# Optimization experiments

Hardware: AMD Instinct MI355X
Metric: run time of the kernel (lower is better)

## Reference

```python
import jax, jax.numpy as jnp
import numpy as np

T, N, D_OBS = 32, 32, 64
HID, HEADS, MEM, N_ACT = 512, 4, 128, 16
SECTIONS = [HEADS * HID, HEADS, HID, 1, HID, HID, HEADS, 1, 1, 3 * HEADS]
XI = sum(SECTIONS)


def setup_inputs() -> dict:
    key = jax.random.key(0)
    ks = jax.random.split(key, 8)
    s = 0.02
    return {
        "inputs": jax.random.normal(ks[0], (T, N, D_OBS), jnp.float32),
        "w_ih": jax.random.normal(ks[1], (3 * HID, D_OBS), jnp.float32) * s,
        "w_hh": jax.random.normal(ks[2], (3 * HID, HID), jnp.float32) * s,
        "b_ih": jnp.zeros((3 * HID,), jnp.float32),
        "b_hh": jnp.zeros((3 * HID,), jnp.float32),
        "Wf": jax.random.normal(ks[3], (XI, HID), jnp.float32) * s,
        "bf": jnp.zeros((XI,), jnp.float32),
        "Wa": jax.random.normal(ks[4], (N_ACT, HID), jnp.float32) * s,
        "ba": jnp.zeros((N_ACT,), jnp.float32),
        "Wc": jax.random.normal(ks[5], (1, HID), jnp.float32) * s,
        "bc": jnp.zeros((1,), jnp.float32),
    }


def reference(inputs, w_ih, w_hh, b_ih, b_hh, Wf, bf, Wa, ba, Wc, bc):
    idx = np.cumsum(SECTIONS)[:-1]
    eps = 1e-8

    def step(carry, x_t):
        h, wr, u, ww, M, p, L = carry
        # --- GRU cell (torch convention) ---
        gi = x_t @ w_ih.T + b_ih
        gh = h @ w_hh.T + b_hh
        ir, iz, inn = jnp.split(gi, 3, axis=-1)
        hr, hz, hn = jnp.split(gh, 3, axis=-1)
        rg = jax.nn.sigmoid(ir + hr)
        zg = jax.nn.sigmoid(iz + hz)
        ng = jnp.tanh(inn + rg * hn)
        h = (1 - zg) * ng + zg * h
        # --- interface vector xi ---
        xi = jax.nn.relu(h) @ Wf.T + bf
        Kr, Br, kw, bw, e, v, F_hat, ga, gw, Pi = jnp.split(xi, idx, axis=-1)
        Kr = Kr.reshape(N, HEADS, HID)
        Br = jax.nn.softplus(Br)                      # [N,H]
        bw = jax.nn.softplus(bw)                      # [N,1]
        e = jax.nn.sigmoid(e)                         # [N,HID] erase
        v_w = v                                       # [N,HID] write vec
        F_hat = jax.nn.sigmoid(F_hat)                 # [N,H] free gates
        ga = jax.nn.sigmoid(ga)                       # [N,1]
        gw = jax.nn.sigmoid(gw)                       # [N,1]
        Pi = jax.nn.softmax(Pi.reshape(N, HEADS, 3), axis=-1)
        # --- memory retention & usage ---
        psi = jnp.prod(1 - F_hat[..., None] * wr, axis=1)          # [N,MEM]
        u = (u + ww - u * ww) * psi
        # --- allocation weighting via usage sort ---
        phi = jnp.argsort(u, axis=-1)
        u_sorted = jnp.take_along_axis(u, phi, axis=-1)
        excl = jnp.concatenate(
            [jnp.ones((N, 1), u.dtype), jnp.cumprod(u_sorted[:, :-1], axis=-1)], axis=-1)
        a_sorted = (1 - u_sorted) * excl
        alloc = jnp.zeros_like(u).at[jnp.arange(N)[:, None], phi].set(a_sorted)
        # --- content-based write weighting ---
        Mn = jnp.sqrt(jnp.sum(M * M, axis=-1))                     # [N,MEM]
        kwn = jnp.sqrt(jnp.sum(kw * kw, axis=-1, keepdims=True))   # [N,1]
        cos_w = jnp.einsum('nmd,nd->nm', M, kw) / (Mn * kwn + eps)
        cw = jax.nn.softmax(bw * cos_w, axis=-1)
        ww = gw * (ga * alloc + (1 - ga) * cw)                     # [N,MEM]
        # --- memory write (erase + add outer products) ---
        M = M * (1 - ww[..., None] * e[:, None, :]) + ww[..., None] * v_w[:, None, :]
        # --- precedence & temporal link matrix ---
        p = (1 - jnp.sum(ww, axis=-1, keepdims=True)) * p + ww
        L = (1 - ww[..., None] - ww[:, None, :]) * L + ww[..., None] * p[:, None, :]
        # --- forward/backward read weights ---
        fwd_w = jnp.einsum('nij,nhj->nhi', L, wr)
        bwd_w = jnp.einsum('nji,nhj->nhi', L, wr)
        # --- content-based read weighting ---
        Mn2 = jnp.sqrt(jnp.sum(M * M, axis=-1))                    # [N,MEM]
        Krn = jnp.sqrt(jnp.sum(Kr * Kr, axis=-1, keepdims=True))   # [N,H,1]
        cos_r = jnp.einsum('nmd,nhd->nhm', M, Kr) / (Mn2[:, None, :] * Krn + eps)
        cr = jax.nn.softmax(Br[..., None] * cos_r, axis=-1)
        wr = Pi[..., 0:1] * bwd_w + Pi[..., 1:2] * cr + Pi[..., 2:3] * fwd_w
        # --- read vectors, actor, critic ---
        r_read = jnp.einsum('nmd,nhm->nd', M, wr)                  # sum over heads -> [N,HID]
        a_probs = jax.nn.softmax(r_read @ Wa.T + ba, axis=-1)      # [N,N_ACT]
        val = h @ Wc.T + bc                                        # [N,1]
        return (h, wr, u, ww, M, p, L), jnp.concatenate([a_probs, val], axis=-1)

    z = jnp.zeros
    carry0 = (z((N, HID)), z((N, HEADS, MEM)), z((N, MEM)), z((N, MEM)),
              z((N, MEM, HID)), z((N, MEM)), z((N, MEM, MEM)))
    _, outs = jax.lax.scan(step, carry0, inputs)
    return outs  # [T, N, N_ACT+1]
```

## Files before the change

kernel.cpp:

```cpp
#include <hip/hip_runtime.h>
#include <math.h>

#define TT 32
#define NB 32
#define DOBS 64
#define HID 512
#define HEADS 4
#define MEM 128
#define NACT 16
#define XID 3607
#define G3 1536

__device__ __forceinline__ float sigm(float x){ return 1.0f/(1.0f+__expf(-x)); }
__device__ __forceinline__ float splus(float x){ return fmaxf(x,0.f) + log1pf(__expf(-fabsf(x))); }

__device__ __forceinline__ float wsum64(float s){
    s += __shfl_xor(s,1); s += __shfl_xor(s,2); s += __shfl_xor(s,4);
    s += __shfl_xor(s,8); s += __shfl_xor(s,16);
    float t = s;
    asm volatile("v_permlane32_swap_b32 %0, %1" : "+v"(s), "+v"(t));
    return s + t;
}
__device__ __forceinline__ float wmax64(float s){
    s = fmaxf(s, __shfl_xor(s,1)); s = fmaxf(s, __shfl_xor(s,2)); s = fmaxf(s, __shfl_xor(s,4));
    s = fmaxf(s, __shfl_xor(s,8)); s = fmaxf(s, __shfl_xor(s,16));
    float t = s;
    asm volatile("v_permlane32_swap_b32 %0, %1" : "+v"(s), "+v"(t));
    return fmaxf(s, t);
}

__global__ __launch_bounds__(256) void k_transpose(const float* __restrict__ src,
                                                   float* __restrict__ dst, int R, int C)
{
    __shared__ float tile[32][33];
    int r0 = blockIdx.x*32, c0 = blockIdx.y*32;
    int tx = threadIdx.x, ty = threadIdx.y;
    #pragma unroll
    for (int yy = 0; yy < 32; yy += 8) {
        int r = r0 + ty + yy, c = c0 + tx;
        if (r < R && c < C) tile[ty+yy][tx] = src[(size_t)r*C + c];
    }
    __syncthreads();
    #pragma unroll
    for (int yy = 0; yy < 32; yy += 8) {
        int c = c0 + ty + yy, r = r0 + tx;
        if (r < R && c < C) dst[(size_t)c*R + r] = tile[tx][ty+yy];
    }
}

__global__ __launch_bounds__(384) void k_gru(
    const float* __restrict__ x,
    const float* __restrict__ wihT,
    const float* __restrict__ whhT,
    const float* __restrict__ b_ih,
    const float* __restrict__ b_hh,
    float* __restrict__ h_all,
    float* hG,
    int* flags)
{
    const int n   = blockIdx.x & 31;
    const int s   = blockIdx.x >> 5;
    const int tid = threadIdx.x;
    const int kq  = tid / 96;
    const int c   = tid % 96;
    const int g   = c >> 5;
    const int r0  = g*512 + s*128 + (c & 31)*4;

    __shared__ float hS[512];
    __shared__ float xS[64];
    __shared__ float4 pI[4][96];
    __shared__ float4 pH[4][96];
    __shared__ float grS[128], gzS[128], giN[128], ghN[128];

    for (int i = tid; i < 512; i += 384) hS[i] = 0.f;

    for (int t = 0; t < TT; ++t) {
        if (tid < 64) xS[tid] = x[((size_t)t*NB + n)*DOBS + tid];
        __syncthreads();
        {
            float4 aI = make_float4(0.f,0.f,0.f,0.f);
            float4 aH = make_float4(0.f,0.f,0.f,0.f);
            const int kx0 = kq*16;
            #pragma unroll 4
            for (int k = kx0; k < kx0+16; ++k) {
                float xv = xS[k];
                float4 w = *(const float4*)(wihT + (size_t)k*G3 + r0);
                aI.x += w.x*xv; aI.y += w.y*xv; aI.z += w.z*xv; aI.w += w.w*xv;
            }
            const int kh0 = kq*128;
            #pragma unroll 4
            for (int k = kh0; k < kh0+128; ++k) {
                float hv = hS[k];
                float4 w = *(const float4*)(whhT + (size_t)k*G3 + r0);
                aH.x += w.x*hv; aH.y += w.y*hv; aH.z += w.z*hv; aH.w += w.w*hv;
            }
            pI[kq][c] = aI; pH[kq][c] = aH;
        }
        __syncthreads();
        {
            const int g2 = tid >> 7, d = tid & 127;
            const int c2 = g2*32 + (d>>2), e = d & 3;
            float AI = 0.f, AH = 0.f;
            #pragma unroll
            for (int q = 0; q < 4; ++q) {
                float4 vi = pI[q][c2], vh = pH[q][c2];
                AI += (e==0)?vi.x:(e==1)?vi.y:(e==2)?vi.z:vi.w;
                AH += (e==0)?vh.x:(e==1)?vh.y:(e==2)?vh.z:vh.w;
            }
            const int rg = g2*512 + s*128 + d;
            AI += b_ih[rg]; AH += b_hh[rg];
            if (g2 == 0)      grS[d] = AI + AH;
            else if (g2 == 1) gzS[d] = AI + AH;
            else              { giN[d] = AI; ghN[d] = AH; }
        }
        __syncthreads();
        if (tid < 128) {
            const int D = s*128 + tid;
            float rg = sigm(grS[tid]);
            float zg = sigm(gzS[tid]);
            float ng = tanhf(giN[tid] + rg*ghN[tid]);
            float hn = (1.f-zg)*ng + zg*hS[D];
            h_all[((size_t)t*NB + n)*HID + D] = hn;
            __hip_atomic_store(&hG[n*HID + D], hn, __ATOMIC_RELAXED, __HIP_MEMORY_SCOPE_AGENT);
        }
        __syncthreads();
        if (t+1 < TT) {
            if (tid == 0) {
                __hip_atomic_fetch_add(&flags[n], 1, __ATOMIC_RELEASE, __HIP_MEMORY_SCOPE_AGENT);
                while (__hip_atomic_load(&flags[n], __ATOMIC_ACQUIRE, __HIP_MEMORY_SCOPE_AGENT) < 4*(t+1)) {
                    __builtin_amdgcn_s_sleep(4);
                }
            }
            __syncthreads();
            for (int i = tid; i < 512; i += 384)
                hS[i] = __hip_atomic_load(&hG[n*HID + i], __ATOMIC_RELAXED, __HIP_MEMORY_SCOPE_AGENT);
        }
    }
}

__global__ __launch_bounds__(256) void k_xi(
    const float* __restrict__ h_all,
    const float* __restrict__ Wf,
    const float* __restrict__ bf,
    float* __restrict__ xi_all)
{
    __shared__ float As[16][132];
    __shared__ float Bs[16][68];
    const int jt = blockIdx.x * 64;
    const int it = blockIdx.y * 128;
    const int tid = threadIdx.x;
    const int lc = tid & 15, lr = tid >> 4;
    const int tx = tid & 15, ty = tid >> 4;
    float acc[8][4] = {};

    for (int k0 = 0; k0 < HID; k0 += 16) {
        #pragma unroll
        for (int s = 0; s < 8; ++s) {
            int i = lr*8 + s;
            As[lc][i] = fmaxf(h_all[(size_t)(it + i)*HID + k0 + lc], 0.f);
        }
        #pragma unroll
        for (int s = 0; s < 4; ++s) {
            int j = lr*4 + s;
            Bs[lc][j] = (jt + j < XID) ? Wf[(size_t)(jt + j)*HID + k0 + lc] : 0.f;
        }
        __syncthreads();
        #pragma unroll
        for (int k = 0; k < 16; ++k) {
            float a[8], b[4];
            #pragma unroll
            for (int u = 0; u < 8; ++u) a[u] = As[k][ty*8+u];
            #pragma unroll
            for (int v = 0; v < 4; ++v) b[v] = Bs[k][tx*4+v];
            #pragma unroll
            for (int u = 0; u < 8; ++u)
                #pragma unroll
                for (int v = 0; v < 4; ++v) acc[u][v] += a[u]*b[v];
        }
        __syncthreads();
    }
    #pragma unroll
    for (int u = 0; u < 8; ++u)
        #pragma unroll
        for (int v = 0; v < 4; ++v) {
            int i = it + ty*8 + u, j = jt + tx*4 + v;
            if (j < XID) xi_all[(size_t)i*XID + j] = acc[u][v] + bf[j];
        }
}

__global__ __launch_bounds__(64) void k_val(
    const float* __restrict__ h_all, const float* __restrict__ Wc,
    const float* __restrict__ bc, float* __restrict__ out)
{
    const int row = blockIdx.x;
    const int lane = threadIdx.x;
    float acc = 0.f;
    for (int d = lane; d < HID; d += 64) acc += h_all[(size_t)row*HID + d]*Wc[d];
    for (int off = 32; off; off >>= 1) acc += __shfl_down(acc, off);
    if (lane == 0) out[(size_t)row*17 + 16] = acc + bc[0];
}

#define LPAD 132
#define SROW 544
#define DYN_FLOATS (128*LPAD + 16*SROW)
#define CIDX(d) ((((d)>>6)*68) + ((d)&63))

__global__ __launch_bounds__(1024) void k_mem(
    const float* __restrict__ xi_all,
    const float* __restrict__ Wa,
    const float* __restrict__ ba,
    float* __restrict__ out)
{
    extern __shared__ __align__(16) float dynS[];
    float* Lm  = dynS;
    float* scr = dynS + 128*LPAD;

    const int n = blockIdx.x;
    const int tid = threadIdx.x;
    const int lane = tid & 63;
    const int wv = tid >> 6;
    const int m8 = tid >> 3;
    const int q8 = tid & 7;

    __shared__ __align__(16) float KrC[4*544];
    __shared__ __align__(16) float kwC[544], eC[544], vC[544];
    __shared__ __align__(16) float wrC[4*136];
    __shared__ __align__(16) float r_S[512];
    __shared__ float dotK_S[4][132], fwd_S[4][132], bwd_S[4][132];
    __shared__ float u_S[128], ww_S[128], p_S[128], cw_S[128], srt_S[128], aS_S[128];
    __shared__ float Mn2_S[128], dw_S[128];
    __shared__ int   rk_S[128];
    __shared__ float wred[16][6];
    __shared__ float scal_S[8];
    __shared__ float PiRaw[12];
    __shared__ float Pi_S[4][3], Br_S[4], KrN_S[4], F_S[4];
    __shared__ float ba_S[16], logit_S[16];

    float4 Mreg[16];
    #pragma unroll
    for (int i = 0; i < 16; ++i) Mreg[i] = make_float4(0.f,0.f,0.f,0.f);

    for (int i = tid; i < 128*LPAD; i += 1024) Lm[i] = 0.f;
    if (tid < 16) ba_S[tid] = ba[tid];
    if (tid < 128) { u_S[tid]=0.f; ww_S[tid]=0.f; p_S[tid]=0.f; Mn2_S[tid]=0.f; }
    if (tid < 512) wrC[(tid>>7)*136 + CIDX(tid&127)] = 0.f;

    float waR[8];
    #pragma unroll
    for (int j = 0; j < 8; ++j) waR[j] = Wa[(wv<<9) + lane + (j<<6)];

    const bool hasEx = (tid >= 1000 && tid < 1023);
    int exIdx = 0;
    if (tid >= 1000 && tid < 1004)      exIdx = 2048 + (tid - 1000);
    else if (tid == 1004)               exIdx = 2564;
    else if (tid >= 1005 && tid < 1023) exIdx = 3589 + (tid - 1005);

    const float* xi0 = xi_all + (size_t)n*XID;
    float pKrA = xi0[tid];
    float pKrB = xi0[1024 + tid];
    float pkw = 0.f, pv = 0.f, pe = 0.f;
    if (tid < 512) { pkw = xi0[2052 + tid]; pv = xi0[3077 + tid]; }
    else           { pe  = xi0[2565 + (tid - 512)]; }
    float pex = hasEx ? xi0[exIdx] : 0.f;
    __syncthreads();

    for (int t = 0; t < TT; ++t) {
        float scv = 0.f, ev2 = 0.f;

        {
            int d = tid & 511, hh = tid >> 9;
            int co = CIDX(d);
            KrC[hh*544 + co]     = pKrA;
            KrC[(2+hh)*544 + co] = pKrB;
        }
        if (tid < 512) { int co = CIDX(tid); kwC[co] = pkw; vC[co] = pv; }
        else { int s2 = tid - 512; int co = CIDX(s2); eC[co] = sigm(pe); }
        if (hasEx) {
            if (tid < 1004)      Br_S[tid-1000] = splus(pex);
            else if (tid==1004)  scal_S[0] = splus(pex);
            else if (tid < 1009) F_S[tid-1005] = sigm(pex);
            else if (tid==1009)  scal_S[1] = sigm(pex);
            else if (tid==1010)  scal_S[2] = sigm(pex);
            else                 PiRaw[tid-1011] = pex;
        }
        {
            float sA = wsum64(pKrA*pKrA);
            float sB = wsum64(pKrB*pKrB);
            float sK = wsum64(pkw*pkw);
            if (lane == 0) { wred[wv][0]=sA; wred[wv][1]=sB; wred[wv][2]=sK; }
        }
        {
            int tn = (t+1 < TT) ? (t+1) : t;
            const float* xin = xi_all + (size_t)(tn*NB + n)*XID;
            pKrA = xin[tid]; pKrB = xin[1024 + tid];
            if (tid < 512) { pkw = xin[2052 + tid]; pv = xin[3077 + tid]; }
            else           { pe  = xin[2565 + (tid - 512)]; }
            if (hasEx) pex = xin[exIdx];
        }
        __syncthreads();

        if (tid < 4) {
            float s = 0.f;
            #pragma unroll
            for (int w = 0; w < 8; ++w) s += wred[(tid&1)*8 + w][tid>>1];
            KrN_S[tid] = sqrtf(s);
        } else if (tid == 4) {
            float s = 0.f;
            #pragma unroll
            for (int w = 0; w < 8; ++w) s += wred[w][2];
            scal_S[3] = sqrtf(s);
        }
        if (tid < 128) {
            int co = CIDX(tid);
            float psi = (1.f - F_S[0]*wrC[co])      * (1.f - F_S[1]*wrC[136+co])
                      * (1.f - F_S[2]*wrC[272+co])  * (1.f - F_S[3]*wrC[408+co]);
            float uu = u_S[tid], w = ww_S[tid];
            u_S[tid] = (uu + w - uu*w)*psi;
        }
        {
            const float* kwp = kwC + q8*68;
            float dw = 0.f;
            #pragma unroll
            for (int c = 0; c < 16; ++c) {
                float4 x = Mreg[c];
                float4 kk = *(const float4*)(kwp + 4*c);
                dw += x.x*kk.x + x.y*kk.y + x.z*kk.z + x.w*kk.w;
            }
            dw += __shfl_xor(dw,1); dw += __shfl_xor(dw,2); dw += __shfl_xor(dw,4);
            if (q8 == 0) dw_S[m8] = dw;
        }
        __syncthreads();

        {
            float um = u_S[m8];
            int rk = 0;
            #pragma unroll
            for (int jj = 0; jj < 16; ++jj) {
                int j = jj*8 + q8;
                float uj = u_S[j];
                rk += (uj < um || (uj == um && j < m8)) ? 1 : 0;
            }
            rk += __shfl_xor(rk,1); rk += __shfl_xor(rk,2); rk += __shfl_xor(rk,4);
            if (q8 == 0) { rk_S[m8] = rk; srt_S[rk] = um; }
        }
        if (tid < 128) {
            float cwv = scal_S[0]*dw_S[tid]/(Mn2_S[tid]*scal_S[3] + 1e-8f);
            cw_S[tid] = cwv;
            float mx = wmax64(cwv);
            if (lane == 0) wred[wv][0] = mx;
        } else if (tid >= 136 && tid < 140) {
            int h = tid - 136;
            float p0 = PiRaw[3*h], p1 = PiRaw[3*h+1], p2 = PiRaw[3*h+2];
            float mx = fmaxf(p0, fmaxf(p1, p2));
            float e0=__expf(p0-mx), e1=__expf(p1-mx), e2=__expf(p2-mx);
            float s = e0+e1+e2;
            Pi_S[h][0]=e0/s; Pi_S[h][1]=e1/s; Pi_S[h][2]=e2/s;
        }
        __syncthreads();

        if (tid < 128) {
            float ev = __expf(cw_S[tid] - fmaxf(wred[0][0], wred[1][0]));
            cw_S[tid] = ev;
            float s = wsum64(ev);
            if (lane == 0) wred[wv][1] = s;
        }
        if (wv == 0) {
            float x0 = srt_S[2*lane], x1 = srt_S[2*lane+1];
            float pp = x0*x1;
            float sc = pp;
            #pragma unroll
            for (int off = 1; off < 64; off <<= 1) {
                float y = __shfl_up(sc, off);
                if (lane >= off) sc *= y;
            }
            float excl = __shfl_up(sc, 1);
            if (lane == 0) excl = 1.f;
            aS_S[2*lane]   = (1.f - x0)*excl;
            aS_S[2*lane+1] = (1.f - x1)*excl*x0;
        }
        __syncthreads();

        if (tid < 128) {
            float cwsum = wred[0][1] + wred[1][1];
            float alloc = aS_S[rk_S[tid]];
            float ga = scal_S[1], gw = scal_S[2];
            float w = gw*(ga*alloc + (1.f-ga)*cw_S[tid]/cwsum);
            ww_S[tid] = w;
            float s = wsum64(w);
            if (lane == 0) wred[wv][0] = s;
        }
        __syncthreads();

        if (tid < 128) {
            float sww = wred[0][0] + wred[1][0];
            p_S[tid] = (1.f - sww)*p_S[tid] + ww_S[tid];
        }
        {
            const int base = q8*68;
            const float* ep  = eC + base;
            const float* vp  = vC + base;
            const float* k0p = KrC + base;
            const float* k1p = KrC + 544 + base;
            const float* k2p = KrC + 1088 + base;
            const float* k3p = KrC + 1632 + base;
            float wwm = ww_S[m8];
            float nrm=0.f, d0=0.f, d1=0.f, d2=0.f, d3=0.f;
            #pragma unroll
            for (int c = 0; c < 16; ++c) {
                float4 x  = Mreg[c];
                float4 ee = *(const float4*)(ep + 4*c);
                float4 vv = *(const float4*)(vp + 4*c);
                x.x = x.x*(1.f - wwm*ee.x) + wwm*vv.x;
                x.y = x.y*(1.f - wwm*ee.y) + wwm*vv.y;
                x.z = x.z*(1.f - wwm*ee.z) + wwm*vv.z;
                x.w = x.w*(1.f - wwm*ee.w) + wwm*vv.w;
                Mreg[c] = x;
                nrm += x.x*x.x + x.y*x.y + x.z*x.z + x.w*x.w;
                float4 k0 = *(const float4*)(k0p + 4*c);
                float4 k1 = *(const float4*)(k1p + 4*c);
                float4 k2 = *(const float4*)(k2p + 4*c);
                float4 k3 = *(const float4*)(k3p + 4*c);
                d0 += x.x*k0.x + x.y*k0.y + x.z*k0.z + x.w*k0.w;
                d1 += x.x*k1.x + x.y*k1.y + x.z*k1.z + x.w*k1.w;
                d2 += x.x*k2.x + x.y*k2.y + x.z*k2.z + x.w*k2.w;
                d3 += x.x*k3.x + x.y*k3.y + x.z*k3.z + x.w*k3.w;
            }
            nrm += __shfl_xor(nrm,1); nrm += __shfl_xor(nrm,2); nrm += __shfl_xor(nrm,4);
            d0  += __shfl_xor(d0,1);  d0  += __shfl_xor(d0,2);  d0  += __shfl_xor(d0,4);
            d1  += __shfl_xor(d1,1);  d1  += __shfl_xor(d1,2);  d1  += __shfl_xor(d1,4);
            d2  += __shfl_xor(d2,1);  d2  += __shfl_xor(d2,2);  d2  += __shfl_xor(d2,4);
            d3  += __shfl_xor(d3,1);  d3  += __shfl_xor(d3,2);  d3  += __shfl_xor(d3,4);
            if (q8 == 4) Mn2_S[m8] = sqrtf(nrm);
            else if (q8 < 4) dotK_S[q8][m8] = (q8==0) ? d0 : ((q8==1) ? d1 : ((q8==2) ? d2 : d3));
        }
        __syncthreads();

        {
            const int j2 = tid & 127, w8 = tid >> 7;
            float wwj = ww_S[j2], pj = p_S[j2];
            float b0=0.f,b1=0.f,b2=0.f,b3=0.f;
            #pragma unroll
            for (int c2 = 0; c2 < 4; ++c2) {
                const int r0 = (w8<<4) + (c2<<2);
                const int bidx = CIDX(r0);
                float4 wwv = *(const float4*)&ww_S[r0];
                float4 w0v = *(const float4*)&wrC[bidx];
                float4 w1v = *(const float4*)&wrC[136+bidx];
                float4 w2v = *(const float4*)&wrC[272+bidx];
                float4 w3v = *(const float4*)&wrC[408+bidx];
                #pragma unroll
                for (int s4 = 0; s4 < 4; ++s4) {
                    int i2 = r0 + s4;
                    float wwi = (s4==0)?wwv.x:(s4==1)?wwv.y:(s4==2)?wwv.z:wwv.w;
                    float lold = Lm[i2*LPAD + j2];
                    float ln = (1.f - wwi - wwj)*lold + wwi*pj;
                    Lm[i2*LPAD + j2] = ln;
                    b0 += ln*((s4==0)?w0v.x:(s4==1)?w0v.y:(s4==2)?w0v.z:w0v.w);
                    b1 += ln*((s4==0)?w1v.x:(s4==1)?w1v.y:(s4==2)?w1v.z:w1v.w);
                    b2 += ln*((s4==0)?w2v.x:(s4==1)?w2v.y:(s4==2)?w2v.z:w2v.w);
                    b3 += ln*((s4==0)?w3v.x:(s4==1)?w3v.y:(s4==2)?w3v.z:w3v.w);
                }
            }
            float* sp = scr + w8*SROW + j2;
            sp[0]=b0; sp[132]=b1; sp[264]=b2; sp[396]=b3;
        }
        __syncthreads();

        if (tid < 512) {
            int h = tid>>7, mm = tid&127;
            float s = 0.f;
            #pragma unroll
            for (int g = 0; g < 8; ++g) s += scr[g*SROW + h*132 + mm];
            bwd_S[h][mm] = s;
        }
        {
            const float* Lr = Lm + m8*LPAD + q8*16;
            const int wb = ((q8>>2)*68) + ((q8&3)<<4);
            float f0=0.f,f1=0.f,f2=0.f,f3=0.f;
            #pragma unroll
            for (int c = 0; c < 4; ++c) {
                float4 lv = *(const float4*)(Lr + 4*c);
                float4 w0 = *(const float4*)&wrC[wb + 4*c];
                float4 w1 = *(const float4*)&wrC[136 + wb + 4*c];
                float4 w2 = *(const float4*)&wrC[272 + wb + 4*c];
                float4 w3 = *(const float4*)&wrC[408 + wb + 4*c];
                f0 += lv.x*w0.x + lv.y*w0.y + lv.z*w0.z + lv.w*w0.w;
                f1 += lv.x*w1.x + lv.y*w1.y + lv.z*w1.z + lv.w*w1.w;
                f2 += lv.x*w2.x + lv.y*w2.y + lv.z*w2.z + lv.w*w2.w;
                f3 += lv.x*w3.x + lv.y*w3.y + lv.z*w3.z + lv.w*w3.w;
            }
            f0 += __shfl_xor(f0,1); f0 += __shfl_xor(f0,2); f0 += __shfl_xor(f0,4);
            f1 += __shfl_xor(f1,1); f1 += __shfl_xor(f1,2); f1 += __shfl_xor(f1,4);
            f2 += __shfl_xor(f2,1); f2 += __shfl_xor(f2,2); f2 += __shfl_xor(f2,4);
            f3 += __shfl_xor(f3,1); f3 += __shfl_xor(f3,2); f3 += __shfl_xor(f3,4);
            if (q8 < 4) fwd_S[q8][m8] = (q8==0) ? f0 : ((q8==1) ? f1 : ((q8==2) ? f2 : f3));
        }
        if (tid < 512) {
            int h = tid>>7, mm = tid&127;
            scv = Br_S[h]*dotK_S[h][mm]/(Mn2_S[mm]*KrN_S[h] + 1e-8f);
            float mxv = wmax64(scv);
            if (lane == 0) wred[wv][0] = mxv;
        }
        __syncthreads();

        if (tid < 512) {
            int h = tid>>7;
            float hmax = fmaxf(wred[2*h][0], wred[2*h+1][0]);
            ev2 = __expf(scv - hmax);
            float s = wsum64(ev2);
            if (lane == 0) wred[wv][1] = s;
        }
        __syncthreads();

        if (tid < 512) {
            int h = tid>>7, mm = tid&127;
            float hsum = wred[2*h][1] + wred[2*h+1][1];
            float cr = ev2/hsum;
            wrC[h*136 + CIDX(mm)] = Pi_S[h][0]*bwd_S[h][mm] + Pi_S[h][1]*cr + Pi_S[h][2]*fwd_S[h][mm];
        }
        __syncthreads();

        {
            const int co = CIDX(m8);
            float srtm = wrC[co] + wrC[136+co] + wrC[272+co] + wrC[408+co];
            float* sp = scr + wv*SROW + q8*68 + ((lane>>5)<<1);
            #pragma unroll
            for (int c = 0; c < 16; ++c) {
                float v0 = srtm*Mreg[c].x;
                float v1 = srtm*Mreg[c].y;
                float v2 = srtm*Mreg[c].z;
                float v3 = srtm*Mreg[c].w;
                asm volatile("v_permlane32_swap_b32 %0, %1" : "+v"(v0), "+v"(v2));
                float A = v0 + v2;
                asm volatile("v_permlane32_swap_b32 %0, %1" : "+v"(v1), "+v"(v3));
                float B = v1 + v3;
                A += __shfl_xor(A, 8); A += __shfl_xor(A, 16);
                B += __shfl_xor(B, 8); B += __shfl_xor(B, 16);
                if ((lane & 31) < 8) *(float2*)(sp + 4*c) = make_float2(A, B);
            }
        }
        __syncthreads();

        if (tid < 512) {
            int off = ((tid>>6)*68) + (tid&63);
            float r = 0.f;
            #pragma unroll
            for (int w = 0; w < 16; ++w) r += scr[w*SROW + off];
            r_S[tid] = r;
        }
        __syncthreads();

        {
            float acc = 0.f;
            #pragma unroll
            for (int j = 0; j < 8; ++j) acc += waR[j]*r_S[lane + (j<<6)];
            acc = wsum64(acc);
            if (lane == 0) logit_S[wv] = acc + ba_S[wv];
        }
        __syncthreads();

        if (tid < 16) {
            float lg = logit_S[tid];
            float mx = lg;
            mx = fmaxf(mx, __shfl_xor(mx,1)); mx = fmaxf(mx, __shfl_xor(mx,2));
            mx = fmaxf(mx, __shfl_xor(mx,4)); mx = fmaxf(mx, __shfl_xor(mx,8));
            float ex2 = __expf(lg - mx);
            float s = ex2;
            s += __shfl_xor(s,1); s += __shfl_xor(s,2);
            s += __shfl_xor(s,4); s += __shfl_xor(s,8);
            out[(size_t)(t*NB + n)*17 + tid] = ex2/s;
        }
    }
}

extern "C" void kernel_launch(void* const* d_in, const int* in_sizes, int n_in,
                              void* d_out, int out_size, void* d_ws, size_t ws_size,
                              hipStream_t stream) {
    const float* inp  = (const float*)d_in[0];
    const float* w_ih = (const float*)d_in[1];
    const float* w_hh = (const float*)d_in[2];
    const float* b_ih = (const float*)d_in[3];
    const float* b_hh = (const float*)d_in[4];
    const float* Wf   = (const float*)d_in[5];
    const float* bf   = (const float*)d_in[6];
    const float* Wa   = (const float*)d_in[7];
    const float* ba   = (const float*)d_in[8];
    const float* Wc   = (const float*)d_in[9];
    const float* bc   = (const float*)d_in[10];
    float* out = (float*)d_out;

    float* ws = (float*)d_ws;
    float* wihT   = ws;
    float* whhT   = ws + 98304;
    float* h_all  = ws + 884736;
    float* xi_all = ws + 1409024;
    float* hG     = ws + 5102592;
    int*   flags  = (int*)(ws + 5119008);

    static int dynset = 0;
    if (!dynset) {
        hipFuncSetAttribute(reinterpret_cast<const void*>(k_mem),
                            hipFuncAttributeMaxDynamicSharedMemorySize,
                            DYN_FLOATS*4);
        dynset = 1;
    }

    hipMemsetAsync(flags, 0, NB*sizeof(int), stream);

    dim3 tb(32, 8);
    k_transpose<<<dim3(48, 2),  tb, 0, stream>>>(w_ih, wihT, G3, DOBS);
    k_transpose<<<dim3(48, 16), tb, 0, stream>>>(w_hh, whhT, G3, HID);
    k_gru<<<NB*4, 384, 0, stream>>>(inp, wihT, whhT, b_ih, b_hh, h_all, hG, flags);
    k_xi<<<dim3(57, 8), 256, 0, stream>>>(h_all, Wf, bf, xi_all);
    k_val<<<TT*NB, 64, 0, stream>>>(h_all, Wc, bc, out);
    k_mem<<<NB, 1024, DYN_FLOATS*4, stream>>>(xi_all, Wa, ba, out);
}
```

Baseline: 1.388 ms.

## Fuse GRU, xi GEMM and memory stages into one persistent kernel with flag pipelining

```diff
diff --git a/kernel.cpp b/kernel.cpp
--- a/kernel.cpp
+++ b/kernel.cpp
@@ -11,8 +11,14 @@
 #define XID 3607
 #define G3 1536
 
+#define NXIJ 10
+#define NXII 8
+
 __device__ __forceinline__ float sigm(float x){ return 1.0f/(1.0f+__expf(-x)); }
 __device__ __forceinline__ float splus(float x){ return fmaxf(x,0.f) + log1pf(__expf(-fabsf(x))); }
+
+#define XLD(p) __hip_atomic_load((p), __ATOMIC_RELAXED, __HIP_MEMORY_SCOPE_AGENT)
+#define XST(p,v) __hip_atomic_store((p), (v), __ATOMIC_RELAXED, __HIP_MEMORY_SCOPE_AGENT)
 
 __device__ __forceinline__ float wsum64(float s){
     s += __shfl_xor(s,1); s += __shfl_xor(s,2); s += __shfl_xor(s,4);
@@ -48,146 +54,6 @@
     }
 }
 
-__global__ __launch_bounds__(384) void k_gru(
-    const float* __restrict__ x,
-    const float* __restrict__ wihT,
-    const float* __restrict__ whhT,
-    const float* __restrict__ b_ih,
-    const float* __restrict__ b_hh,
-    float* __restrict__ h_all,
-    float* hG,
-    int* flags)
-{
-    const int n   = blockIdx.x & 31;
-    const int s   = blockIdx.x >> 5;
-    const int tid = threadIdx.x;
-    const int kq  = tid / 96;
-    const int c   = tid % 96;
-    const int g   = c >> 5;
-    const int r0  = g*512 + s*128 + (c & 31)*4;
-
-    __shared__ float hS[512];
-    __shared__ float xS[64];
-    __shared__ float4 pI[4][96];
-    __shared__ float4 pH[4][96];
-    __shared__ float grS[128], gzS[128], giN[128], ghN[128];
-
-    for (int i = tid; i < 512; i += 384) hS[i] = 0.f;
-
-    for (int t = 0; t < TT; ++t) {
-        if (tid < 64) xS[tid] = x[((size_t)t*NB + n)*DOBS + tid];
-        __syncthreads();
-        {
-            float4 aI = make_float4(0.f,0.f,0.f,0.f);
-            float4 aH = make_float4(0.f,0.f,0.f,0.f);
-            const int kx0 = kq*16;
-            #pragma unroll 4
-            for (int k = kx0; k < kx0+16; ++k) {
-                float xv = xS[k];
-                float4 w = *(const float4*)(wihT + (size_t)k*G3 + r0);
-                aI.x += w.x*xv; aI.y += w.y*xv; aI.z += w.z*xv; aI.w += w.w*xv;
-            }
-            const int kh0 = kq*128;
-            #pragma unroll 4
-            for (int k = kh0; k < kh0+128; ++k) {
-                float hv = hS[k];
-                float4 w = *(const float4*)(whhT + (size_t)k*G3 + r0);
-                aH.x += w.x*hv; aH.y += w.y*hv; aH.z += w.z*hv; aH.w += w.w*hv;
-            }
-            pI[kq][c] = aI; pH[kq][c] = aH;
-        }
-        __syncthreads();
-        {
-            const int g2 = tid >> 7, d = tid & 127;
-            const int c2 = g2*32 + (d>>2), e = d & 3;
-            float AI = 0.f, AH = 0.f;
-            #pragma unroll
-            for (int q = 0; q < 4; ++q) {
-                float4 vi = pI[q][c2], vh = pH[q][c2];
-                AI += (e==0)?vi.x:(e==1)?vi.y:(e==2)?vi.z:vi.w;
-                AH += (e==0)?vh.x:(e==1)?vh.y:(e==2)?vh.z:vh.w;
-            }
-            const int rg = g2*512 + s*128 + d;
-            AI += b_ih[rg]; AH += b_hh[rg];
-            if (g2 == 0)      grS[d] = AI + AH;
-            else if (g2 == 1) gzS[d] = AI + AH;
-            else              { giN[d] = AI; ghN[d] = AH; }
-        }
-        __syncthreads();
-        if (tid < 128) {
-            const int D = s*128 + tid;
-            float rg = sigm(grS[tid]);
-            float zg = sigm(gzS[tid]);
-            float ng = tanhf(giN[tid] + rg*ghN[tid]);
-            float hn = (1.f-zg)*ng + zg*hS[D];
-            h_all[((size_t)t*NB + n)*HID + D] = hn;
-            __hip_atomic_store(&hG[n*HID + D], hn, __ATOMIC_RELAXED, __HIP_MEMORY_SCOPE_AGENT);
-        }
-        __syncthreads();
-        if (t+1 < TT) {
-            if (tid == 0) {
-                __hip_atomic_fetch_add(&flags[n], 1, __ATOMIC_RELEASE, __HIP_MEMORY_SCOPE_AGENT);
-                while (__hip_atomic_load(&flags[n], __ATOMIC_ACQUIRE, __HIP_MEMORY_SCOPE_AGENT) < 4*(t+1)) {
-                    __builtin_amdgcn_s_sleep(4);
-                }
-            }
-            __syncthreads();
-            for (int i = tid; i < 512; i += 384)
-                hS[i] = __hip_atomic_load(&hG[n*HID + i], __ATOMIC_RELAXED, __HIP_MEMORY_SCOPE_AGENT);
-        }
-    }
-}
-
-__global__ __launch_bounds__(256) void k_xi(
-    const float* __restrict__ h_all,
-    const float* __restrict__ Wf,
-    const float* __restrict__ bf,
-    float* __restrict__ xi_all)
-{
-    __shared__ float As[16][132];
-    __shared__ float Bs[16][68];
-    const int jt = blockIdx.x * 64;
-    const int it = blockIdx.y * 128;
-    const int tid = threadIdx.x;
-    const int lc = tid & 15, lr = tid >> 4;
-    const int tx = tid & 15, ty = tid >> 4;
-    float acc[8][4] = {};
-
-    for (int k0 = 0; k0 < HID; k0 += 16) {
-        #pragma unroll
-        for (int s = 0; s < 8; ++s) {
-            int i = lr*8 + s;
-            As[lc][i] = fmaxf(h_all[(size_t)(it + i)*HID + k0 + lc], 0.f);
-        }
-        #pragma unroll
-        for (int s = 0; s < 4; ++s) {
-            int j = lr*4 + s;
-            Bs[lc][j] = (jt + j < XID) ? Wf[(size_t)(jt + j)*HID + k0 + lc] : 0.f;
-        }
-        __syncthreads();
-        #pragma unroll
-        for (int k = 0; k < 16; ++k) {
-            float a[8], b[4];
-            #pragma unroll
-            for (int u = 0; u < 8; ++u) a[u] = As[k][ty*8+u];
-            #pragma unroll
-            for (int v = 0; v < 4; ++v) b[v] = Bs[k][tx*4+v];
-            #pragma unroll
-            for (int u = 0; u < 8; ++u)
-                #pragma unroll
-                for (int v = 0; v < 4; ++v) acc[u][v] += a[u]*b[v];
-        }
-        __syncthreads();
-    }
-    #pragma unroll
-    for (int u = 0; u < 8; ++u)
-        #pragma unroll
-        for (int v = 0; v < 4; ++v) {
-            int i = it + ty*8 + u, j = jt + tx*4 + v;
-            if (j < XID) xi_all[(size_t)i*XID + j] = acc[u][v] + bf[j];
-        }
-}
-
 __global__ __launch_bounds__(64) void k_val(
     const float* __restrict__ h_all, const float* __restrict__ Wc,
     const float* __restrict__ bc, float* __restrict__ out)
@@ -205,18 +71,181 @@
 #define DYN_FLOATS (128*LPAD + 16*SROW)
 #define CIDX(d) ((((d)>>6)*68) + ((d)&63))
 
-__global__ __launch_bounds__(1024) void k_mem(
-    const float* __restrict__ xi_all,
+__global__ __launch_bounds__(1024) void k_fused(
+    const float* __restrict__ x,
+    const float* __restrict__ wihT,
+    const float* __restrict__ whhT,
+    const float* __restrict__ b_ih,
+    const float* __restrict__ b_hh,
+    float* h_all,
+    const float* __restrict__ Wf,
+    const float* __restrict__ bf,
+    float* xi_all,
     const float* __restrict__ Wa,
     const float* __restrict__ ba,
-    float* __restrict__ out)
+    float* __restrict__ out,
+    float* hG,
+    int* flagsN,
+    int* gstep,
+    int* xidone)
 {
     extern __shared__ __align__(16) float dynS[];
+    const int bid = blockIdx.x;
+    const int tid = threadIdx.x;
+
+    if (bid >= 32 && bid < 160) {
+        const int g = bid - 32;
+        const int n = g & 31, s = g >> 5;
+        float* hS = dynS;
+        float* xS = dynS + 512;
+        float* pI = dynS + 576;
+        float* pH = dynS + 2112;
+        float* grS = dynS + 3648;
+        float* gzS = dynS + 3776;
+        float* giN = dynS + 3904;
+        float* ghN = dynS + 4032;
+
+        const int kq = tid / 96;
+        const int c  = tid % 96;
+        const int gg = c >> 5;
+        const int r0 = gg*512 + s*128 + (c & 31)*4;
+
+        for (int i = tid; i < 512; i += 1024) hS[i] = 0.f;
+
+        for (int t = 0; t < TT; ++t) {
+            if (tid < 64) xS[tid] = x[((size_t)t*NB + n)*DOBS + tid];
+            __syncthreads();
+            if (tid < 384) {
+                float4 aI = make_float4(0.f,0.f,0.f,0.f);
+                float4 aH = make_float4(0.f,0.f,0.f,0.f);
+                const int kx0 = kq*16;
+                #pragma unroll 4
+                for (int k = kx0; k < kx0+16; ++k) {
+                    float xv = xS[k];
+                    float4 w = *(const float4*)(wihT + (size_t)k*G3 + r0);
+                    aI.x += w.x*xv; aI.y += w.y*xv; aI.z += w.z*xv; aI.w += w.w*xv;
+                }
+                const int kh0 = kq*128;
+                #pragma unroll 4
+                for (int k = kh0; k < kh0+128; ++k) {
+                    float hv = hS[k];
+                    float4 w = *(const float4*)(whhT + (size_t)k*G3 + r0);
+                    aH.x += w.x*hv; aH.y += w.y*hv; aH.z += w.z*hv; aH.w += w.w*hv;
+                }
+                *(float4*)&pI[(kq*96 + c)*4] = aI;
+                *(float4*)&pH[(kq*96 + c)*4] = aH;
+            }
+            __syncthreads();
+            if (tid < 384) {
+                const int g2 = tid >> 7, d = tid & 127;
+                const int c2 = g2*32 + (d>>2), e = d & 3;
+                float AI = 0.f, AH = 0.f;
+                #pragma unroll
+                for (int q = 0; q < 4; ++q) {
+                    AI += pI[(q*96 + c2)*4 + e];
+                    AH += pH[(q*96 + c2)*4 + e];
+                }
+                const int rg = g2*512 + s*128 + d;
+                AI += b_ih[rg]; AH += b_hh[rg];
+                if (g2 == 0)      grS[d] = AI + AH;
+                else if (g2 == 1) gzS[d] = AI + AH;
+                else              { giN[d] = AI; ghN[d] = AH; }
+            }
+            __syncthreads();
+            if (tid < 128) {
+                const int D = s*128 + tid;
+                float rg = sigm(grS[tid]);
+                float zg = sigm(gzS[tid]);
+                float ng = tanhf(giN[tid] + rg*ghN[tid]);
+                float hn = (1.f-zg)*ng + zg*hS[D];
+                XST(&h_all[((size_t)t*NB + n)*HID + D], hn);
+                XST(&hG[n*HID + D], hn);
+            }
+            __syncthreads();
+            if (tid == 0) {
+                __hip_atomic_fetch_add(gstep, 1, __ATOMIC_RELEASE, __HIP_MEMORY_SCOPE_AGENT);
+                if (t+1 < TT) {
+                    __hip_atomic_fetch_add(&flagsN[n], 1, __ATOMIC_RELEASE, __HIP_MEMORY_SCOPE_AGENT);
+                    while (__hip_atomic_load(&flagsN[n], __ATOMIC_ACQUIRE, __HIP_MEMORY_SCOPE_AGENT) < 4*(t+1)) {
+                        __builtin_amdgcn_s_sleep(4);
+                    }
+                }
+            }
+            if (t+1 < TT) {
+                __syncthreads();
+                for (int i = tid; i < 512; i += 1024)
+                    hS[i] = XLD(&hG[n*HID + i]);
+            }
+        }
+        return;
+    }
+
+    if (bid >= 160) {
+        const int q2 = bid - 160;
+        const int jtile = q2 % NXIJ, itile = q2 / NXIJ;
+        const int it = itile*128, jt = jtile*384;
+        float* As = dynS;
+        float* Bs = dynS + 16*132;
+        const int q  = tid >> 8;
+        const int t8 = tid & 255;
+        const int lc = t8 & 15, lr = t8 >> 4;
+        const int tx = t8 & 15, ty = t8 >> 4;
+        const int i2 = tid >> 4;
+
+        if (tid == 0) {
+            while (__hip_atomic_load(gstep, __ATOMIC_ACQUIRE, __HIP_MEMORY_SCOPE_AGENT) < 128*(4*itile+4)) {
+                __builtin_amdgcn_s_sleep(8);
+            }
+        }
+        __syncthreads();
+
+        float acc[8][6] = {};
+        for (int k0 = 0; k0 < HID; k0 += 16) {
+            #pragma unroll
+            for (int s = 0; s < 2; ++s) {
+                int i = i2*2 + s;
+                float hv = XLD(&h_all[(size_t)(it + i)*HID + k0 + lc]);
+                As[lc*132 + i] = fmaxf(hv, 0.f);
+            }
+            #pragma unroll
+            for (int s = 0; s < 6; ++s) {
+                int j = lr*6 + s;
+                int col = jt + q*96 + j;
+                Bs[lc*400 + q*100 + j] = (col < XID) ? Wf[(size_t)col*HID + k0 + lc] : 0.f;
+            }
+            __syncthreads();
+            #pragma unroll
+            for (int k = 0; k < 16; ++k) {
+                float a[8], b[6];
+                #pragma unroll
+                for (int u = 0; u < 8; ++u) a[u] = As[k*132 + ty*8 + u];
+                #pragma unroll
+                for (int v = 0; v < 6; ++v) b[v] = Bs[k*400 + q*100 + tx*6 + v];
+                #pragma unroll
+                for (int u = 0; u < 8; ++u)
+                    #pragma unroll
+                    for (int v = 0; v < 6; ++v) acc[u][v] += a[u]*b[v];
+            }
+            __syncthreads();
+        }
+        #pragma unroll
+        for (int u = 0; u < 8; ++u)
+            #pragma unroll
+            for (int v = 0; v < 6; ++v) {
+                int i = it + ty*8 + u, j = jt + q*96 + tx*6 + v;
+                if (j < XID) XST(&xi_all[(size_t)i*XID + j], acc[u][v] + bf[j]);
+            }
+        __syncthreads();
+        if (tid == 0)
+            __hip_atomic_fetch_add(&xidone[itile], 1, __ATOMIC_RELEASE, __HIP_MEMORY_SCOPE_AGENT);
+        return;
+    }
+
+    {
     float* Lm  = dynS;
     float* scr = dynS + 128*LPAD;
 
-    const int n = blockIdx.x;
-    const int tid = threadIdx.x;
+    const int n = bid;
     const int lane = tid & 63;
     const int wv = tid >> 6;
     const int m8 = tid >> 3;
@@ -255,14 +284,20 @@
     else if (tid == 1004)               exIdx = 2564;
     else if (tid >= 1005 && tid < 1023) exIdx = 3589 + (tid - 1005);
 
+    if (tid == 0) {
+        while (__hip_atomic_load(&xidone[0], __ATOMIC_ACQUIRE, __HIP_MEMORY_SCOPE_AGENT) < NXIJ) {
+            __builtin_amdgcn_s_sleep(8);
+        }
+    }
+    __syncthreads();
+
     const float* xi0 = xi_all + (size_t)n*XID;
-    float pKrA = xi0[tid];
-    float pKrB = xi0[1024 + tid];
+    float pKrA = XLD(&xi0[tid]);
+    float pKrB = XLD(&xi0[1024 + tid]);
     float pkw = 0.f, pv = 0.f, pe = 0.f;
-    if (tid < 512) { pkw = xi0[2052 + tid]; pv = xi0[3077 + tid]; }
-    else           { pe  = xi0[2565 + (tid - 512)]; }
-    float pex = hasEx ? xi0[exIdx] : 0.f;
-    __syncthreads();
+    if (tid < 512) { pkw = XLD(&xi0[2052 + tid]); pv = XLD(&xi0[3077 + tid]); }
+    else           { pe  = XLD(&xi0[2565 + (tid - 512)]); }
+    float pex = hasEx ? XLD(&xi0[exIdx]) : 0.f;
 
     for (int t = 0; t < TT; ++t) {
         float scv = 0.f, ev2 = 0.f;
@@ -291,11 +326,19 @@
         }
         {
             int tn = (t+1 < TT) ? (t+1) : t;
+            if (t+1 < TT && ((t+1) & 3) == 0) {
+                if (tid == 0) {
+                    while (__hip_atomic_load(&xidone[(t+1)>>2], __ATOMIC_ACQUIRE, __HIP_MEMORY_SCOPE_AGENT) < NXIJ) {
+                        __builtin_amdgcn_s_sleep(8);
+                    }
+                }
+                __syncthreads();
+            }
             const float* xin = xi_all + (size_t)(tn*NB + n)*XID;
-            pKrA = xin[tid]; pKrB = xin[1024 + tid];
-            if (tid < 512) { pkw = xin[2052 + tid]; pv = xin[3077 + tid]; }
-            else           { pe  = xin[2565 + (tid - 512)]; }
-            if (hasEx) pex = xin[exIdx];
+            pKrA = XLD(&xin[tid]); pKrB = XLD(&xin[1024 + tid]);
+            if (tid < 512) { pkw = XLD(&xin[2052 + tid]); pv = XLD(&xin[3077 + tid]); }
+            else           { pe  = XLD(&xin[2565 + (tid - 512)]); }
+            if (hasEx) pex = XLD(&xin[exIdx]);
         }
         __syncthreads();
 
@@ -322,9 +365,9 @@
             float dw = 0.f;
             #pragma unroll
             for (int c = 0; c < 16; ++c) {
-                float4 x = Mreg[c];
+                float4 xx = Mreg[c];
                 float4 kk = *(const float4*)(kwp + 4*c);
-                dw += x.x*kk.x + x.y*kk.y + x.z*kk.z + x.w*kk.w;
+                dw += xx.x*kk.x + xx.y*kk.y + xx.z*kk.z + xx.w*kk.w;
             }
             dw += __shfl_xor(dw,1); dw += __shfl_xor(dw,2); dw += __shfl_xor(dw,4);
             if (q8 == 0) dw_S[m8] = dw;
@@ -407,23 +450,23 @@
             float nrm=0.f, d0=0.f, d1=0.f, d2=0.f, d3=0.f;
             #pragma unroll
             for (int c = 0; c < 16; ++c) {
-                float4 x  = Mreg[c];
+                float4 xx = Mreg[c];
                 float4 ee = *(const float4*)(ep + 4*c);
                 float4 vv = *(const float4*)(vp + 4*c);
-                x.x = x.x*(1.f - wwm*ee.x) + wwm*vv.x;
-                x.y = x.y*(1.f - wwm*ee.y) + wwm*vv.y;
-                x.z = x.z*(1.f - wwm*ee.z) + wwm*vv.z;
-                x.w = x.w*(1.f - wwm*ee.w) + wwm*vv.w;
-                Mreg[c] = x;
-                nrm += x.x*x.x + x.y*x.y + x.z*x.z + x.w*x.w;
+                xx.x = xx.x*(1.f - wwm*ee.x) + wwm*vv.x;
+                xx.y = xx.y*(1.f - wwm*ee.y) + wwm*vv.y;
+                xx.z = xx.z*(1.f - wwm*ee.z) + wwm*vv.z;
+                xx.w = xx.w*(1.f - wwm*ee.w) + wwm*vv.w;
+                Mreg[c] = xx;
+                nrm += xx.x*xx.x + xx.y*xx.y + xx.z*xx.z + xx.w*xx.w;
                 float4 k0 = *(const float4*)(k0p + 4*c);
                 float4 k1 = *(const float4*)(k1p + 4*c);
                 float4 k2 = *(const float4*)(k2p + 4*c);
                 float4 k3 = *(const float4*)(k3p + 4*c);
-                d0 += x.x*k0.x + x.y*k0.y + x.z*k0.z + x.w*k0.w;
-                d1 += x.x*k1.x + x.y*k1.y + x.z*k1.z + x.w*k1.w;
-                d2 += x.x*k2.x + x.y*k2.y + x.z*k2.z + x.w*k2.w;
-                d3 += x.x*k3.x + x.y*k3.y + x.z*k3.z + x.w*k3.w;
+                d0 += xx.x*k0.x + xx.y*k0.y + xx.z*k0.z + xx.w*k0.w;
+                d1 += xx.x*k1.x + xx.y*k1.y + xx.z*k1.z + xx.w*k1.w;
+                d2 += xx.x*k2.x + xx.y*k2.y + xx.z*k2.z + xx.w*k2.w;
+                d3 += xx.x*k3.x + xx.y*k3.y + xx.z*k3.z + xx.w*k3.w;
             }
             nrm += __shfl_xor(nrm,1); nrm += __shfl_xor(nrm,2); nrm += __shfl_xor(nrm,4);
             d0  += __shfl_xor(d0,1);  d0  += __shfl_xor(d0,2);  d0  += __shfl_xor(d0,4);
@@ -441,16 +484,16 @@
             float b0=0.f,b1=0.f,b2=0.f,b3=0.f;
             #pragma unroll
             for (int c2 = 0; c2 < 4; ++c2) {
-                const int r0 = (w8<<4) + (c2<<2);
-                const int bidx = CIDX(r0);
-                float4 wwv = *(const float4*)&ww_S[r0];
+                const int rr0 = (w8<<4) + (c2<<2);
+                const int bidx = CIDX(rr0);
+                float4 wwv = *(const float4*)&ww_S[rr0];
                 float4 w0v = *(const float4*)&wrC[bidx];
                 float4 w1v = *(const float4*)&wrC[136+bidx];
                 float4 w2v = *(const float4*)&wrC[272+bidx];
                 float4 w3v = *(const float4*)&wrC[408+bidx];
                 #pragma unroll
                 for (int s4 = 0; s4 < 4; ++s4) {
-                    int i2 = r0 + s4;
+                    int i2 = rr0 + s4;
                     float wwi = (s4==0)?wwv.x:(s4==1)?wwv.y:(s4==2)?wwv.z:wwv.w;
                     float lold = Lm[i2*LPAD + j2];
                     float ln = (1.f - wwi - wwj)*lold + wwi*pj;
@@ -570,6 +613,7 @@
             s += __shfl_xor(s,4); s += __shfl_xor(s,8);
             out[(size_t)(t*NB + n)*17 + tid] = ex2/s;
         }
+    }
     }
 }
 
@@ -595,23 +639,25 @@
     float* h_all  = ws + 884736;
     float* xi_all = ws + 1409024;
     float* hG     = ws + 5102592;
-    int*   flags  = (int*)(ws + 5119008);
+    int*   flagsN = (int*)(ws + 5119008);
+    int*   gstep  = flagsN + 32;
+    int*   xidone = gstep + 1;
 
     static int dynset = 0;
     if (!dynset) {
-        hipFuncSetAttribute(reinterpret_cast<const void*>(k_mem),
+        hipFuncSetAttribute(reinterpret_cast<const void*>(k_fused),
                             hipFuncAttributeMaxDynamicSharedMemorySize,
                             DYN_FLOATS*4);
         dynset = 1;
     }
 
-    hipMemsetAsync(flags, 0, NB*sizeof(int), stream);
+    hipMemsetAsync(flagsN, 0, 48*sizeof(int), stream);
 
     dim3 tb(32, 8);
     k_transpose<<<dim3(48, 2),  tb, 0, stream>>>(w_ih, wihT, G3, DOBS);
     k_transpose<<<dim3(48, 16), tb, 0, stream>>>(w_hh, whhT, G3, HID);
-    k_gru<<<NB*4, 384, 0, stream>>>(inp, wihT, whhT, b_ih, b_hh, h_all, hG, flags);
-    k_xi<<<dim3(57, 8), 256, 0, stream>>>(h_all, Wf, bf, xi_all);
+    k_fused<<<32 + 128 + NXII*NXIJ, 1024, DYN_FLOATS*4, stream>>>(
+        inp, wihT, whhT, b_ih, b_hh, h_all, Wf, bf, xi_all, Wa, ba, out,
+        hG, flagsN, gstep, xidone);
     k_val<<<TT*NB, 64, 0, stream>>>(h_all, Wc, bc, out);
-    k_mem<<<NB, 1024, DYN_FLOATS*4, stream>>>(xi_all, Wa, ba, out);
 }
```

New measurement: 1.785 ms. 28.6% more time.
